# Kernel tuning notes

Hardware: AMD Instinct MI355X
Metric: run time of the kernel (lower is better)

## Reference

```python
import jax, jax.numpy as jnp
import numpy as np

N, C, NUM_GROUPS = 4_194_304, 16, 8


def setup_inputs() -> dict:
    key = jax.random.key(0)
    k1, k2, k3 = jax.random.split(key, 3)
    input_ = jax.random.normal(k1, (N, C), dtype=jnp.float32)
    target = jax.random.randint(k2, (N,), 0, C, dtype=jnp.int64) if jax.config.jax_enable_x64 else jax.random.randint(k2, (N,), 0, C, dtype=jnp.int32)
    group = jax.random.randint(k3, (N,), 0, NUM_GROUPS, dtype=jnp.int32)
    return {"input_": input_, "target": target, "group": group}


def reference(input_, target, group):
    # gather input_[i, target[i]] and take |1 - .|
    err = jnp.abs(1.0 - jnp.take_along_axis(input_, target[:, None].astype(jnp.int32), axis=1)[:, 0])  # [N]
    # per-group mean == L1-row-normalized one-hot matmul in the original
    sums = jax.ops.segment_sum(err, group, num_segments=NUM_GROUPS)               # [G]
    counts = jax.ops.segment_sum(jnp.ones_like(err), group, num_segments=NUM_GROUPS)
    means = jnp.where(counts > 0, sums / jnp.maximum(counts, 1.0), 0.0)           # empty group -> 0 (F.normalize eps behavior)
    loss_target_value = 0.5
    return jnp.abs(loss_target_value - means.mean())
```

## Files before the change

### kernel.cpp

```cpp
#include <hip/hip_runtime.h>

#define N_ELEMS 4194304
#define C_DIM 16
#define G_NUM 8


__global__ __launch_bounds__(256) void berl_partial(
    const float* __restrict__ input_,
    const int*   __restrict__ target,
    const int*   __restrict__ group,
    float*        __restrict__ g_sums,
    unsigned int* __restrict__ g_counts)
{
    __shared__ float        s_sums[G_NUM];
    __shared__ unsigned int s_counts[G_NUM];
    const int tid = threadIdx.x;
    if (tid < G_NUM) { s_sums[tid] = 0.0f; s_counts[tid] = 0u; }
    __syncthreads();

    float sums[G_NUM];
    float cnts[G_NUM];
#pragma unroll
    for (int g = 0; g < G_NUM; ++g) { sums[g] = 0.0f; cnts[g] = 0.0f; }

    const int4* t4 = (const int4*)target;
    const int4* g4 = (const int4*)group;
    const int n4     = N_ELEMS / 4;
    const int stride = gridDim.x * blockDim.x;

    for (int i = blockIdx.x * blockDim.x + tid; i < n4; i += stride) {
        int4 t = t4[i];
        int4 g = g4[i];
        const int base = i * (4 * C_DIM);
        float e0 = fabsf(1.0f - __builtin_nontemporal_load(&input_[base + 0 * C_DIM + t.x]));
        float e1 = fabsf(1.0f - __builtin_nontemporal_load(&input_[base + 1 * C_DIM + t.y]));
        float e2 = fabsf(1.0f - __builtin_nontemporal_load(&input_[base + 2 * C_DIM + t.z]));
        float e3 = fabsf(1.0f - __builtin_nontemporal_load(&input_[base + 3 * C_DIM + t.w]));
#pragma unroll
        for (int k = 0; k < G_NUM; ++k) {
            sums[k] += (g.x == k) ? e0 : 0.0f;
            sums[k] += (g.y == k) ? e1 : 0.0f;
            sums[k] += (g.z == k) ? e2 : 0.0f;
            sums[k] += (g.w == k) ? e3 : 0.0f;
            cnts[k] += (g.x == k) ? 1.0f : 0.0f;
            cnts[k] += (g.y == k) ? 1.0f : 0.0f;
            cnts[k] += (g.z == k) ? 1.0f : 0.0f;
            cnts[k] += (g.w == k) ? 1.0f : 0.0f;
        }
    }

#pragma unroll
    for (int k = 0; k < G_NUM; ++k) {
        atomicAdd(&s_sums[k], sums[k]);
        atomicAdd(&s_counts[k], (unsigned int)cnts[k]);
    }
    __syncthreads();

    if (tid < G_NUM) {
        atomicAdd(&g_sums[tid], s_sums[tid]);
        atomicAdd(&g_counts[tid], s_counts[tid]);
    }
}

__global__ void berl_final(const float* __restrict__ g_sums,
                           const unsigned int* __restrict__ g_counts,
                           float* __restrict__ out)
{
    if (threadIdx.x == 0 && blockIdx.x == 0) {
        float acc = 0.0f;
#pragma unroll
        for (int g = 0; g < G_NUM; ++g) {
            float c = (float)g_counts[g];
            float m = (c > 0.0f) ? (g_sums[g] / fmaxf(c, 1.0f)) : 0.0f;
            acc += m;
        }
        out[0] = fabsf(0.5f - acc / (float)G_NUM);
    }
}

extern "C" void kernel_launch(void* const* d_in, const int* in_sizes, int n_in,
                              void* d_out, int out_size, void* d_ws, size_t ws_size,
                              hipStream_t stream) {
    const float* input_ = (const float*)d_in[0];
    const int*   target = (const int*)d_in[1];
    const int*   group  = (const int*)d_in[2];
    float* out = (float*)d_out;

    float*        g_sums   = (float*)d_ws;
    unsigned int* g_counts = (unsigned int*)((char*)d_ws + G_NUM * sizeof(float));

    hipMemsetAsync(d_ws, 0, G_NUM * (sizeof(float) + sizeof(unsigned int)), stream);

    dim3 block(256);
    dim3 grid(2048);
    berl_partial<<<grid, block, 0, stream>>>(input_, target, group, g_sums, g_counts);
    berl_final<<<1, 64, 0, stream>>>(g_sums, g_counts, out);
}
```

Before: 416.4 us.

## Stage input rows through LDS with coalesced float4 loads instead of scattered gathers

Replaces per-element scattered gathers from global memory with block-wide coalesced float4 loads of 256 full rows into shared memory, then picks the target column from LDS. The goal is fewer, wider memory transactions. In exchange it adds two block barriers per stage with no load/compute overlap inside a block, and drops the nontemporal load hints.

```diff
diff --git a/kernel.cpp b/kernel.cpp
--- a/kernel.cpp
+++ b/kernel.cpp
@@ -3,6 +3,8 @@
 #define N_ELEMS 4194304
 #define C_DIM 16
 #define G_NUM 8
+#define ROWS_PER_STAGE 256
+#define NUM_STAGES (N_ELEMS / ROWS_PER_STAGE)
 
 
 __global__ __launch_bounds__(256) void berl_partial(
@@ -12,41 +14,40 @@
     float*        __restrict__ g_sums,
     unsigned int* __restrict__ g_counts)
 {
+    __shared__ float4       s_rows[ROWS_PER_STAGE * 4];
     __shared__ float        s_sums[G_NUM];
     __shared__ unsigned int s_counts[G_NUM];
+
     const int tid = threadIdx.x;
     if (tid < G_NUM) { s_sums[tid] = 0.0f; s_counts[tid] = 0u; }
-    __syncthreads();
 
     float sums[G_NUM];
     float cnts[G_NUM];
 #pragma unroll
-    for (int g = 0; g < G_NUM; ++g) { sums[g] = 0.0f; cnts[g] = 0.0f; }
+    for (int k = 0; k < G_NUM; ++k) { sums[k] = 0.0f; cnts[k] = 0.0f; }
 
-    const int4* t4 = (const int4*)target;
-    const int4* g4 = (const int4*)group;
-    const int n4     = N_ELEMS / 4;
-    const int stride = gridDim.x * blockDim.x;
+    const float4* __restrict__ in4 = (const float4*)input_;
 
-    for (int i = blockIdx.x * blockDim.x + tid; i < n4; i += stride) {
-        int4 t = t4[i];
-        int4 g = g4[i];
-        const int base = i * (4 * C_DIM);
-        float e0 = fabsf(1.0f - __builtin_nontemporal_load(&input_[base + 0 * C_DIM + t.x]));
-        float e1 = fabsf(1.0f - __builtin_nontemporal_load(&input_[base + 1 * C_DIM + t.y]));
-        float e2 = fabsf(1.0f - __builtin_nontemporal_load(&input_[base + 2 * C_DIM + t.z]));
-        float e3 = fabsf(1.0f - __builtin_nontemporal_load(&input_[base + 3 * C_DIM + t.w]));
+    for (int s = blockIdx.x; s < NUM_STAGES; s += gridDim.x) {
+        const int row0 = s * ROWS_PER_STAGE;
+        const int f4_base = row0 * 4;
+
+#pragma unroll
+        for (int q = 0; q < 4; ++q) {
+            s_rows[tid + 256 * q] = in4[f4_base + tid + 256 * q];
+        }
+        __syncthreads();
+
+        const int t = target[row0 + tid];
+        const int g = group[row0 + tid];
+        const float v = ((const float*)s_rows)[tid * C_DIM + t];
+        const float e = fabsf(1.0f - v);
 #pragma unroll
         for (int k = 0; k < G_NUM; ++k) {
-            sums[k] += (g.x == k) ? e0 : 0.0f;
-            sums[k] += (g.y == k) ? e1 : 0.0f;
-            sums[k] += (g.z == k) ? e2 : 0.0f;
-            sums[k] += (g.w == k) ? e3 : 0.0f;
-            cnts[k] += (g.x == k) ? 1.0f : 0.0f;
-            cnts[k] += (g.y == k) ? 1.0f : 0.0f;
-            cnts[k] += (g.z == k) ? 1.0f : 0.0f;
-            cnts[k] += (g.w == k) ? 1.0f : 0.0f;
+            sums[k] += (g == k) ? e : 0.0f;
+            cnts[k] += (g == k) ? 1.0f : 0.0f;
         }
+        __syncthreads();
     }
 
 #pragma unroll
```

After: 446.5 us. +7.2%, slower.
